# Optimization experiments

Measured on AMD Instinct MI355X. Metric: run time of the kernel, lower is better.

Reference implementation:

```python
import jax, jax.numpy as jnp
import numpy as np

B, OUT, IN, G = 256, 256, 256, 8


def setup_inputs() -> dict:
    key = jax.random.key(0)
    k1, k2, k3, k4 = jax.random.split(key, 4)
    x = jax.random.normal(k1, (B, IN), dtype=jnp.float32)
    # xavier-like scale for spline_weight
    spline_weight = jax.random.normal(k2, (OUT, IN, G), dtype=jnp.float32) * 0.06
    # scaler initialized to ones in torch; use positive values near 1 to exercise the exp
    spline_scaler = jax.random.uniform(k3, (OUT, IN), dtype=jnp.float32, minval=0.5, maxval=1.5)
    # base_activation initialized to zeros in torch; small random to exercise the residual path
    base_activation = jax.random.normal(k4, (OUT, IN), dtype=jnp.float32) * 0.02
    grid = jnp.linspace(-2.0, 2.0, G, dtype=jnp.float32)
    return {
        "x": x,
        "spline_weight": spline_weight,
        "spline_scaler": spline_scaler,
        "base_activation": base_activation,
        "grid": grid,
    }


def reference(x, spline_weight, spline_scaler, base_activation, grid):
    # x: (B, IN) -> out: (B, OUT)
    xn = jnp.tanh(x)                                        # (B, IN)
    # RBF-like basis: exp(-|tanh(x) - grid| * scaler), shape (B, OUT, IN, G)
    dist = jnp.abs(xn[:, None, :, None] - grid[None, None, None, :])  # (B, 1, IN, G)
    basis = jnp.exp(-dist * spline_scaler[None, :, :, None])          # (B, OUT, IN, G)
    # reduce over grid dim with the spline weights
    spline_out = jnp.einsum('boig,oig->boi', basis, spline_weight)    # (B, OUT, IN)
    out = spline_out + base_activation[None, :, :] * xn[:, None, :]   # (B, OUT, IN)
    return jnp.sum(out, axis=-1)                                      # (B, OUT)
```

## Files before the change

kernel.cpp:

```cpp
#include <hip/hip_runtime.h>


#define B_   256
#define OUT_ 256
#define IN_  256
#define G_   8
#define NK   5
#define BT   2
#define OT   64

__global__ void kan_prep(const float* __restrict__ x,
                         const float* __restrict__ w,
                         const float* __restrict__ sc,
                         const float* __restrict__ ba,
                         const float* __restrict__ grid,
                         float2* __restrict__ xnk,
                         float2* __restrict__ sbt,
                         float2* __restrict__ T)
{
    float g[G_];
#pragma unroll
    for (int j = 0; j < G_; ++j) g[j] = grid[j];

    {
        const int idx = blockIdx.x * 256 + threadIdx.x;
        const float xn = tanhf(x[idx]);
        int k = 0;
#pragma unroll
        for (int j = 0; j < G_; ++j) k += (g[j] <= xn) ? 1 : 0;
        k = min(max(k, 2), 6) - 2;
        const int row = k * IN_ + (idx & (IN_ - 1));
        xnk[idx] = make_float2(xn, __int_as_float(row));
    }

    {
        const int i = blockIdx.x;
        const int o = threadIdx.x;
        const int base = o * IN_ + i;
        const float s  = sc[base];
        const float bv = ba[base];

        float Ep[G_], Em[G_];
#pragma unroll
        for (int j = 0; j < G_; ++j) {
            const float wv = w[base * G_ + j];
            const float t  = s * g[j];
            Ep[j] = wv * __expf(t);
            Em[j] = wv * __expf(-t);
        }
#pragma unroll
        for (int kk = 0; kk < NK; ++kk) {
            const int k = kk + 2;
            float A = 0.f, Bv = 0.f;
#pragma unroll
            for (int j = 0; j < G_; ++j) {
                if (j < k) A += Ep[j]; else Bv += Em[j];
            }
            T[(kk * IN_ + i) * OUT_ + o] = make_float2(A, Bv);
        }
        sbt[i * OUT_ + o] = make_float2(s * 1.44269504088896340736f, bv);
    }
}

__global__ __launch_bounds__(256, 8) void kan_main(
        const float2* __restrict__ xnk,
        const float2* __restrict__ sbt,
        const float2* __restrict__ T,
        float* __restrict__ out)
{
    const int lane = threadIdx.x & 63;
    const int igrp = threadIdx.x >> 6;
    const int ot   = blockIdx.x & 3;
    const int bg   = blockIdx.x >> 2;
    const int o    = ot * OT + lane;
    const int b0   = bg * BT;

    __shared__ float2 sxk[BT * IN_];
    __shared__ float  sacc[4][BT][OT];

    for (int t = threadIdx.x; t < BT * IN_; t += 256)
        sxk[t] = xnk[b0 * IN_ + t];
    __syncthreads();

    float acc[BT];
#pragma unroll
    for (int bb = 0; bb < BT; ++bb) acc[bb] = 0.f;

    const int i0 = igrp * 64;
    for (int ii = 0; ii < 64; ++ii) {
        const int i = i0 + ii;
        const float2 sb = sbt[i * OUT_ + o];
#pragma unroll
        for (int bb = 0; bb < BT; ++bb) {
            const float2 xk = sxk[bb * IN_ + i];
            const float xn  = xk.x;
            const int   row = __float_as_int(xk.y);
            const float2 rec = T[(row << 8) + o];
            const float t = sb.x * xn;
            float a = fmaf(sb.y, xn, acc[bb]);
            a       = fmaf(exp2f(-t), rec.x, a);
            acc[bb] = fmaf(exp2f(t),  rec.y, a);
        }
    }

#pragma unroll
    for (int bb = 0; bb < BT; ++bb) sacc[igrp][bb][lane] = acc[bb];
    __syncthreads();

    if (threadIdx.x < BT * OT) {
        const int bb = threadIdx.x >> 6;
        const int l  = threadIdx.x & 63;
        const float s = sacc[0][bb][l] + sacc[1][bb][l]
                      + sacc[2][bb][l] + sacc[3][bb][l];
        out[(b0 + bb) * OUT_ + ot * OT + l] = s;
    }
}

extern "C" void kernel_launch(void* const* d_in, const int* in_sizes, int n_in,
                              void* d_out, int out_size, void* d_ws, size_t ws_size,
                              hipStream_t stream)
{
    const float* x    = (const float*)d_in[0];
    const float* w    = (const float*)d_in[1];
    const float* sc   = (const float*)d_in[2];
    const float* ba   = (const float*)d_in[3];
    const float* grid = (const float*)d_in[4];
    float* out = (float*)d_out;

    char* ws = (char*)d_ws;
    float2* xnk = (float2*)(ws);
    float2* sbt = (float2*)(ws + 512 * 1024);
    float2* T   = (float2*)(ws + 1024 * 1024);

    kan_prep<<<IN_, 256, 0, stream>>>(x, w, sc, ba, grid, xnk, sbt, T);
    kan_main<<<(B_ / BT) * (OUT_ / OT), 256, 0, stream>>>(xnk, sbt, T, out);
}
```

Measured before the change: 83.67 us.

## Tile T table in shared memory per input chunk and split-K with a reduce kernel

The main kernel now assigns each block a 16-input by 64-output slab for 32 batch rows and stages the needed T, scale/base and x/k entries in shared memory. This replaces the per-element gathers from global T with LDS lookups reused across batch rows. Partial sums over input chunks go to a workspace buffer, and a new reduce kernel adds the 16 partials. The cost is an extra kernel launch, a partial-buffer write and read, and lower occupancy because of the larger LDS footprint.

Result: slower. 86.82 us (+3.8%).

```diff
diff --git a/kernel.cpp b/kernel.cpp
--- a/kernel.cpp
+++ b/kernel.cpp
@@ -6,17 +6,20 @@
 #define IN_  256
 #define G_   8
 #define NK   5
-#define BT   2
+#define BG   32
+#define ICH  16
+#define NIC  (IN_/ICH)
 #define OT   64
 
-__global__ void kan_prep(const float* __restrict__ x,
-                         const float* __restrict__ w,
-                         const float* __restrict__ sc,
-                         const float* __restrict__ ba,
-                         const float* __restrict__ grid,
-                         float2* __restrict__ xnk,
-                         float2* __restrict__ sbt,
-                         float2* __restrict__ T)
+__global__ __launch_bounds__(256) void kan_prep(
+        const float* __restrict__ x,
+        const float* __restrict__ w,
+        const float* __restrict__ sc,
+        const float* __restrict__ ba,
+        const float* __restrict__ grid,
+        float2* __restrict__ xnk,
+        float2* __restrict__ sbt,
+        float2* __restrict__ T)
 {
     float g[G_];
 #pragma unroll
@@ -29,8 +32,7 @@
 #pragma unroll
         for (int j = 0; j < G_; ++j) k += (g[j] <= xn) ? 1 : 0;
         k = min(max(k, 2), 6) - 2;
-        const int row = k * IN_ + (idx & (IN_ - 1));
-        xnk[idx] = make_float2(xn, __int_as_float(row));
+        xnk[idx] = make_float2(xn, (float)k);
     }
 
     {
@@ -62,58 +64,75 @@
     }
 }
 
-__global__ __launch_bounds__(256, 8) void kan_main(
+__global__ __launch_bounds__(256, 2) void kan_main(
         const float2* __restrict__ xnk,
         const float2* __restrict__ sbt,
         const float2* __restrict__ T,
-        float* __restrict__ out)
+        float* __restrict__ partial)
 {
     const int lane = threadIdx.x & 63;
-    const int igrp = threadIdx.x >> 6;
-    const int ot   = blockIdx.x & 3;
-    const int bg   = blockIdx.x >> 2;
-    const int o    = ot * OT + lane;
-    const int b0   = bg * BT;
+    const int w    = threadIdx.x >> 6;
+    const int slab = blockIdx.x & 63;
+    const int bg   = blockIdx.x >> 6;
+    const int ot   = slab & 3;
+    const int ic   = slab >> 2;
+    const int o0   = ot * OT;
+    const int i0   = ic * ICH;
+    const int b0   = bg * BG;
 
-    __shared__ float2 sxk[BT * IN_];
-    __shared__ float  sacc[4][BT][OT];
+    __shared__ float2 sT[NK * ICH * OT];
+    __shared__ float2 sSB[ICH * OT];
+    __shared__ float2 sXK[BG * ICH];
 
-    for (int t = threadIdx.x; t < BT * IN_; t += 256)
-        sxk[t] = xnk[b0 * IN_ + t];
+    for (int idx = threadIdx.x; idx < NK * ICH * OT; idx += 256) {
+        const int kk = idx >> 10;
+        const int rem = idx & 1023;
+        const int ii = rem >> 6, ol = rem & 63;
+        sT[idx] = T[(kk * IN_ + i0 + ii) * OUT_ + o0 + ol];
+    }
+    for (int idx = threadIdx.x; idx < ICH * OT; idx += 256) {
+        const int ii = idx >> 6, ol = idx & 63;
+        sSB[idx] = sbt[(i0 + ii) * OUT_ + o0 + ol];
+    }
+    for (int idx = threadIdx.x; idx < BG * ICH; idx += 256) {
+        const int bb = idx >> 4, ii = idx & 15;
+        const float2 v = xnk[(b0 + bb) * IN_ + i0 + ii];
+        sXK[idx] = make_float2(v.x, __int_as_float(((int)v.y) << 10));
+    }
     __syncthreads();
 
-    float acc[BT];
+    float acc[8];
 #pragma unroll
-    for (int bb = 0; bb < BT; ++bb) acc[bb] = 0.f;
+    for (int bb = 0; bb < 8; ++bb) acc[bb] = 0.f;
 
-    const int i0 = igrp * 64;
-    for (int ii = 0; ii < 64; ++ii) {
-        const int i = i0 + ii;
-        const float2 sb = sbt[i * OUT_ + o];
+    const int wb = w * 8;
+    for (int ii = 0; ii < ICH; ++ii) {
+        const float2 sb = sSB[ii * OT + lane];
+        const int il = ii * OT + lane;
 #pragma unroll
-        for (int bb = 0; bb < BT; ++bb) {
-            const float2 xk = sxk[bb * IN_ + i];
-            const float xn  = xk.x;
-            const int   row = __float_as_int(xk.y);
-            const float2 rec = T[(row << 8) + o];
-            const float t = sb.x * xn;
-            float a = fmaf(sb.y, xn, acc[bb]);
+        for (int bb = 0; bb < 8; ++bb) {
+            const float2 xk = sXK[(wb + bb) * ICH + ii];
+            const float2 rec = sT[__float_as_int(xk.y) + il];
+            const float t = sb.x * xk.x;
+            float a = fmaf(sb.y, xk.x, acc[bb]);
             a       = fmaf(exp2f(-t), rec.x, a);
             acc[bb] = fmaf(exp2f(t),  rec.y, a);
         }
     }
 
+    float* p = partial + ((size_t)ic * B_ + b0 + wb) * OUT_ + o0 + lane;
 #pragma unroll
-    for (int bb = 0; bb < BT; ++bb) sacc[igrp][bb][lane] = acc[bb];
-    __syncthreads();
+    for (int bb = 0; bb < 8; ++bb) p[bb * OUT_] = acc[bb];
+}
 
-    if (threadIdx.x < BT * OT) {
-        const int bb = threadIdx.x >> 6;
-        const int l  = threadIdx.x & 63;
-        const float s = sacc[0][bb][l] + sacc[1][bb][l]
-                      + sacc[2][bb][l] + sacc[3][bb][l];
-        out[(b0 + bb) * OUT_ + ot * OT + l] = s;
-    }
+__global__ __launch_bounds__(256) void kan_reduce(
+        const float* __restrict__ partial, float* __restrict__ out)
+{
+    const int idx = blockIdx.x * 256 + threadIdx.x;
+    float s = 0.f;
+#pragma unroll
+    for (int c = 0; c < NIC; ++c) s += partial[c * (B_ * OUT_) + idx];
+    out[idx] = s;
 }
 
 extern "C" void kernel_launch(void* const* d_in, const int* in_sizes, int n_in,
@@ -131,7 +150,9 @@
     float2* xnk = (float2*)(ws);
     float2* sbt = (float2*)(ws + 512 * 1024);
     float2* T   = (float2*)(ws + 1024 * 1024);
+    float*  partial = (float*)(ws + 1024 * 1024 + (size_t)NK * IN_ * OUT_ * sizeof(float2));
 
     kan_prep<<<IN_, 256, 0, stream>>>(x, w, sc, ba, grid, xnk, sbt, T);
-    kan_main<<<(B_ / BT) * (OUT_ / OT), 256, 0, stream>>>(xnk, sbt, T, out);
+    kan_main<<<64 * (B_ / BG), 256, 0, stream>>>(xnk, sbt, T, partial);
+    kan_reduce<<<(B_ * OUT_) / 256, 256, 0, stream>>>(partial, out);
 }
```
